# Performance work log

Measured on AMD Instinct MI355X. Metric: run time of the kernel, lower is better.

## Reference

```python
import jax, jax.numpy as jnp
import numpy as np

H, C = 4, 32            # num_heads, hidden_channels per head
HC = H * C
SLOPE_ATT = 0.2         # GATv2Conv negative_slope default
SLOPE_OUT = 0.01        # F.leaky_relu default

N_HOST, N_VM, N_JOB, N_SWITCH = 50000, 100000, 200000, 5000
IN_DIM = 64
E_HS, E_VH, E_JV = 200000, 400000, 800000


def _gatv2(x_src, x_dst, Wl, bl, Wr, br, att, bias, src, dst, n_dst):
    # PyG GATv2Conv (bipartite): lin_l on source, lin_r on destination
    xl = (x_src @ Wl + bl).reshape(-1, H, C)             # [Ns,H,C]
    xr = (x_dst @ Wr + br).reshape(-1, H, C)             # [Nd,H,C]
    e = jax.nn.leaky_relu(xl[src] + xr[dst], SLOPE_ATT)  # [E,H,C]
    logits = jnp.einsum('ehc,hc->eh', e, att)            # [E,H]
    m = jax.ops.segment_max(logits, dst, num_segments=n_dst)
    ex = jnp.exp(logits - m[dst])
    denom = jax.ops.segment_sum(ex, dst, num_segments=n_dst)
    alpha = ex / denom[dst]                              # scatter-softmax grouped by dst
    out = jax.ops.segment_sum(xl[src] * alpha[..., None], dst, num_segments=n_dst)
    return out.reshape(n_dst, HC) + bias, alpha


def setup_inputs() -> dict:
    key = jax.random.key(0)
    ks = iter(jax.random.split(key, 64))
    f32 = jnp.float32
    def randn(shape, scale=1.0):
        return jax.random.normal(next(ks), shape, dtype=f32) * scale
    sw = 1.0 / np.sqrt(IN_DIM)
    sa = 1.0 / np.sqrt(C)
    inp = {
        'x_host': randn((N_HOST, IN_DIM)),
        'x_vm': randn((N_VM, IN_DIM)),
        'x_job': randn((N_JOB, IN_DIM)),
        'x_switch': randn((N_SWITCH, IN_DIM)),
        'e_hs_src': jax.random.randint(next(ks), (E_HS,), 0, N_HOST),
        'e_hs_dst': jax.random.randint(next(ks), (E_HS,), 0, N_SWITCH),
        'e_vh_src': jax.random.randint(next(ks), (E_VH,), 0, N_VM),
        'e_vh_dst': jax.random.randint(next(ks), (E_VH,), 0, N_HOST),
        'e_jv_src': jax.random.randint(next(ks), (E_JV,), 0, N_JOB),
        'e_jv_dst': jax.random.randint(next(ks), (E_JV,), 0, N_VM),
    }
    for rel in ('hs', 'vh', 'jv'):
        inp['Wl_' + rel] = randn((IN_DIM, HC), sw)
        inp['bl_' + rel] = jnp.zeros((HC,), f32)
        inp['Wr_' + rel] = randn((IN_DIM, HC), sw)
        inp['br_' + rel] = jnp.zeros((HC,), f32)
        inp['att_' + rel] = randn((H, C), sa)
        inp['bias_' + rel] = jnp.zeros((HC,), f32)
    for nt in ('host', 'vm', 'job', 'switch'):
        inp['W_' + nt] = randn((HC, 1), 1.0 / np.sqrt(HC))
        inp['b_' + nt] = jnp.zeros((1,), f32)
    return inp


def reference(x_host, x_vm, x_job, x_switch,
              e_hs_src, e_hs_dst, e_vh_src, e_vh_dst, e_jv_src, e_jv_dst,
              Wl_hs, bl_hs, Wr_hs, br_hs, att_hs, bias_hs,
              Wl_vh, bl_vh, Wr_vh, br_vh, att_vh, bias_vh,
              Wl_jv, bl_jv, Wr_jv, br_jv, att_jv, bias_jv,
              W_host, b_host, W_vm, b_vm, W_job, b_job, W_switch, b_switch):
    out_switch, a_hs = _gatv2(x_host, x_switch, Wl_hs, bl_hs, Wr_hs, br_hs,
                              att_hs, bias_hs, e_hs_src, e_hs_dst, x_switch.shape[0])
    out_host, a_vh = _gatv2(x_vm, x_host, Wl_vh, bl_vh, Wr_vh, br_vh,
                            att_vh, bias_vh, e_vh_src, e_vh_dst, x_host.shape[0])
    out_vm, a_jv = _gatv2(x_job, x_vm, Wl_jv, bl_jv, Wr_jv, br_jv,
                          att_jv, bias_jv, e_jv_src, e_jv_dst, x_vm.shape[0])
    # each dst type receives exactly one relation; stack+sum is identity here
    h_host = jax.nn.leaky_relu(out_host, SLOPE_OUT)
    h_vm = jax.nn.leaky_relu(out_vm, SLOPE_OUT)
    h_switch = jax.nn.leaky_relu(out_switch, SLOPE_OUT)
    h_job = jnp.zeros((x_job.shape[0], HC), x_job.dtype)  # job has no incoming edges
    s_host = jax.nn.sigmoid(h_host @ W_host + b_host)
    s_vm = jax.nn.sigmoid(h_vm @ W_vm + b_vm)
    s_job = jax.nn.sigmoid(h_job @ W_job + b_job)
    s_switch = jax.nn.sigmoid(h_switch @ W_switch + b_switch)
    scores = jnp.concatenate([s_host, s_vm, s_job, s_switch], axis=0)
    return scores, a_hs, a_vh, a_jv
```

## Files before the change

kernel.cpp:

```cpp
#include <hip/hip_runtime.h>
#include <hip/hip_fp16.h>


#define SLOPE_ATT 0.2f
#define SLOPE_OUT 0.01f

typedef _Float16 half8_t __attribute__((ext_vector_type(8)));
typedef _Float16 v2h_t __attribute__((ext_vector_type(2)));
typedef float float4_t __attribute__((ext_vector_type(4)));

__device__ __forceinline__ float dot8(half8_t a, half8_t b, float acc) {
    v2h_t a0 = __builtin_shufflevector(a, a, 0, 1);
    v2h_t a1 = __builtin_shufflevector(a, a, 2, 3);
    v2h_t a2 = __builtin_shufflevector(a, a, 4, 5);
    v2h_t a3 = __builtin_shufflevector(a, a, 6, 7);
    v2h_t b0 = __builtin_shufflevector(b, b, 0, 1);
    v2h_t b1 = __builtin_shufflevector(b, b, 2, 3);
    v2h_t b2 = __builtin_shufflevector(b, b, 4, 5);
    v2h_t b3 = __builtin_shufflevector(b, b, 6, 7);
    acc = __builtin_amdgcn_fdot2(a0, b0, acc, false);
    acc = __builtin_amdgcn_fdot2(a1, b1, acc, false);
    acc = __builtin_amdgcn_fdot2(a2, b2, acc, false);
    acc = __builtin_amdgcn_fdot2(a3, b3, acc, false);
    return acc;
}

struct WSrc { const float* W[6]; };

__global__ __launch_bounds__(256) void init_wt_kernel(
    int* __restrict__ head, int ptot, WSrc wsrc, __half* __restrict__ Wt) {
    int i = blockIdx.x * 256 + threadIdx.x;
    if (i < ptot) {
        head[i] = -1;
    } else {
        int r = i - ptot;
        if (r < 6 * 8192) {
            int j = r >> 13;
            int rr = r & 8191;
            int n = rr >> 6, k = rr & 63;
            Wt[r] = (__half)wsrc.W[j][k * 128 + n];
        }
    }
}

__device__ __forceinline__ void gemm_tile_mfma(
    const float* __restrict__ X, const __half* __restrict__ Wt,
    const float* __restrict__ bb, __half* __restrict__ Y,
    int M, int block_row, __half (*sY)[16][136]) {
    const int lane = threadIdx.x & 63;
    const int wv = threadIdx.x >> 6;
    const int m0 = block_row + wv * 16;
    const int mr = lane & 15;
    const int quad = lane >> 4;
    const int gr = m0 + mr;
    const bool valid = gr < M;

    half8_t a0 = {}, a1 = {};
    float4 xa = {}, xb = {}, xc = {}, xd = {};
    if (valid) {
        const float4* xp = (const float4*)(X + (size_t)gr * 64 + quad * 8);
        xa = xp[0]; xb = xp[1];
        const float4* xq = (const float4*)(X + (size_t)gr * 64 + 32 + quad * 8);
        xc = xq[0]; xd = xq[1];
    }

    half8_t wb0[8], wb1[8];
    float bv[8];
#pragma unroll
    for (int t = 0; t < 8; t++) {
        const __half* wb = Wt + ((size_t)(t * 16 + mr)) * 64 + quad * 8;
        wb0[t] = *(const half8_t*)wb;
        wb1[t] = *(const half8_t*)(wb + 32);
        bv[t] = bb[t * 16 + mr];
    }

    a0[0] = (_Float16)xa.x; a0[1] = (_Float16)xa.y;
    a0[2] = (_Float16)xa.z; a0[3] = (_Float16)xa.w;
    a0[4] = (_Float16)xb.x; a0[5] = (_Float16)xb.y;
    a0[6] = (_Float16)xb.z; a0[7] = (_Float16)xb.w;
    a1[0] = (_Float16)xc.x; a1[1] = (_Float16)xc.y;
    a1[2] = (_Float16)xc.z; a1[3] = (_Float16)xc.w;
    a1[4] = (_Float16)xd.x; a1[5] = (_Float16)xd.y;
    a1[6] = (_Float16)xd.z; a1[7] = (_Float16)xd.w;

#pragma unroll
    for (int t = 0; t < 8; t++) {
        float4_t c = {0.f, 0.f, 0.f, 0.f};
        c = __builtin_amdgcn_mfma_f32_16x16x32_f16(a0, wb0[t], c, 0, 0, 0);
        c = __builtin_amdgcn_mfma_f32_16x16x32_f16(a1, wb1[t], c, 0, 0, 0);
        int ocol = t * 16 + mr;
        int lrow = quad * 4;
#pragma unroll
        for (int r = 0; r < 4; r++)
            sY[wv][lrow + r][ocol] = (__half)(c[r] + bv[t]);
    }

    const int rl = lane >> 4;
    const int c8 = (lane & 15) * 8;
#pragma unroll
    for (int i = 0; i < 4; i++) {
        int row = i * 4 + rl;
        int gr2 = m0 + row;
        if (gr2 < M) {
            half8_t v = *(const half8_t*)&sY[wv][row][c8];
            *(half8_t*)&Y[(size_t)gr2 * 128 + c8] = v;
        }
    }
}

__device__ __forceinline__ void link_work(
    int linkId, int linkBlocks,
    const int* __restrict__ d0, const int* __restrict__ s0,
    const int* __restrict__ d1, const int* __restrict__ s1,
    const int* __restrict__ d2, const int* __restrict__ s2,
    int* __restrict__ head, int2* __restrict__ nxt,
    int E0, int E1, int E2, int pb1, int pb2) {
    int i = linkId * 256 + threadIdx.x;
    int Etot = E0 + E1 + E2;
    int stride = linkBlocks * 256;
    for (; i < Etot; i += stride) {
        int le, slot; const int* sp;
        if (i < E0)           { le = i;           slot = d0[le];       sp = s0; }
        else if (i < E0 + E1) { le = i - E0;      slot = pb1 + d1[le]; sp = s1; }
        else                  { le = i - E0 - E1; slot = pb2 + d2[le]; sp = s2; }
        int old = atomicExch(&head[slot], le);
        nxt[i] = make_int2(old, sp[le]);
    }
}

struct GemmJobs {
    const float* X[6]; const float* b[6]; __half* Y[6];
    int M[6]; int base[7];
};

__global__ __launch_bounds__(256) void mega_gemm_link_kernel(
    GemmJobs j, const __half* __restrict__ Wt, int s, int L,
    const int* __restrict__ d0, const int* __restrict__ s0,
    const int* __restrict__ d1, const int* __restrict__ s1,
    const int* __restrict__ d2, const int* __restrict__ s2,
    int* __restrict__ head, int2* __restrict__ nxt,
    int E0, int E1, int E2, int pb1, int pb2) {
    __shared__ __half sY[4][16][136];
    int b = blockIdx.x;
    int q = b / s;
    bool onGridline = (b - q * s) == 0;
    if (onGridline && q < L) {
        link_work(q, L, d0, s0, d1, s1, d2, s2, head, nxt, E0, E1, E2, pb1, pb2);
    } else {
        int before = q + (onGridline ? 0 : 1);
        if (before > L) before = L;
        int g = b - before;
        int k = 0;
        while (g >= j.base[k + 1]) k++;
        gemm_tile_mfma(j.X[k], Wt + (size_t)k * 8192, j.b[k], j.Y[k], j.M[k],
                       (g - j.base[k]) * 64, sY);
    }
}

struct AggJob {
    const __half* xl; const __half* xr; const float* att;
    const int* head; const int2* nxt;
    float* ex; float* dn;
    const float* bias; const float* Wn; const float* bn; float* scores;
    int Nd;
};
struct AggJobs { AggJob r[3]; int base[4]; };

__global__ __launch_bounds__(256) void agg3_kernel(AggJobs aj) {
    int b = blockIdx.x;
    int k = 0;
    while (b >= aj.base[k + 1]) k++;
    AggJob J = aj.r[k];

    const int l = threadIdx.x & 63;
    const int wv = threadIdx.x >> 6;
    const int li = l & 7;
    const int g = l >> 3;
    const int dbase = ((b - aj.base[k]) * 4 + wv) * 8;
    const int d = dbase + g;
    if (dbase >= J.Nd) return;
    const bool dok = d < J.Nd;
    const int h = li >> 1;

    half8_t xr0 = {}, xr1 = {};
    if (dok) {
        const half8_t* xrp = (const half8_t*)(J.xr + (size_t)d * 128) + li * 2;
        xr0 = xrp[0]; xr1 = xrp[1];
    }
    half8_t at0, at1;
    {
        const float* ap = J.att + li * 16;
#pragma unroll
        for (int i = 0; i < 8; i++) {
            at0[i] = (_Float16)ap[i];
            at1[i] = (_Float16)ap[8 + i];
        }
    }
    const half8_t sl8 = {(_Float16)SLOPE_ATT, (_Float16)SLOPE_ATT,
                         (_Float16)SLOPE_ATT, (_Float16)SLOPE_ATT,
                         (_Float16)SLOPE_ATT, (_Float16)SLOPE_ATT,
                         (_Float16)SLOPE_ATT, (_Float16)SLOPE_ATT};

    float acc[16] = {};
    float ssum = 0.f;

    int e = dok ? J.head[d] : -1;
    const bool any = (e >= 0);

    while (__any(e >= 0)) {
        bool act = (e >= 0);
        int2 ns = act ? J.nxt[e] : make_int2(-1, 0);
        half8_t x0 = {}, x1 = {};
        if (act) {
            const half8_t* xp = (const half8_t*)(J.xl + (size_t)ns.y * 128) + li * 2;
            x0 = xp[0]; x1 = xp[1];
        }
        if (act) {
            half8_t v0 = x0 + xr0;
            half8_t v1 = x1 + xr1;
            half8_t lk0 = __builtin_elementwise_max(v0, v0 * sl8);
            half8_t lk1 = __builtin_elementwise_max(v1, v1 * sl8);
            float p = dot8(lk1, at1, dot8(lk0, at0, 0.f));
            p += __shfl_xor(p, 1);
            float w = __expf(p);
            if ((li & 1) == 0) J.ex[(size_t)e * 4 + h] = w;
            ssum += w;
#pragma unroll
            for (int i = 0; i < 8; i++) {
                acc[i]     += w * (float)x0[i];
                acc[8 + i] += w * (float)x1[i];
            }
        }
        e = act ? ns.x : -1;
    }

    if (dok && (li & 1) == 0) J.dn[(size_t)d * 4 + h] = ssum;

    float rr = any ? 1.f / ssum : 0.f;
    float pr = 0.f;
    if (dok) {
        const float* bp = J.bias + li * 16;
        const float* wp = J.Wn + li * 16;
#pragma unroll
        for (int i = 0; i < 16; i++) {
            float o = acc[i] * rr + bp[i];
            o = o > 0.f ? o : SLOPE_OUT * o;
            pr += o * wp[i];
        }
    }
    pr += __shfl_xor(pr, 1);
    pr += __shfl_xor(pr, 2);
    pr += __shfl_xor(pr, 4);
    if (dok && li == 0)
        J.scores[d] = 1.f / (1.f + __expf(-(pr + J.bn[0])));
}

__global__ __launch_bounds__(256) void alpha_job_kernel(
    float* __restrict__ ex,
    const int* __restrict__ d0, const int* __restrict__ d1,
    const int* __restrict__ d2,
    const float* __restrict__ dn,
    int E0, int E1, int E2, int pb1, int pb2, int ab,
    const float* __restrict__ bjob, float* __restrict__ sjob, int NJ) {
    int b = blockIdx.x;
    if (b < ab) {
        int i = b * 256 + threadIdx.x;
        int tot = (E0 + E1 + E2) * 4;
        if (i >= tot) return;
        int e = i >> 2, h = i & 3;
        int d;
        if (e < E0)           d = d0[e];
        else if (e < E0 + E1) d = pb1 + d1[e - E0];
        else                  d = pb2 + d2[e - E0 - E1];
        ex[i] = ex[i] / dn[(size_t)d * 4 + h];
    } else {
        int i = (b - ab) * 256 + threadIdx.x;
        if (i < NJ) sjob[i] = 1.f / (1.f + __expf(-bjob[0]));
    }
}


extern "C" void kernel_launch(void* const* d_in, const int* in_sizes, int n_in,
                              void* d_out, int out_size, void* d_ws, size_t ws_size,
                              hipStream_t stream) {
    const float* x_host   = (const float*)d_in[0];
    const float* x_vm     = (const float*)d_in[1];
    const float* x_job    = (const float*)d_in[2];
    const float* x_switch = (const float*)d_in[3];
    const int* e_hs_src = (const int*)d_in[4];
    const int* e_hs_dst = (const int*)d_in[5];
    const int* e_vh_src = (const int*)d_in[6];
    const int* e_vh_dst = (const int*)d_in[7];
    const int* e_jv_src = (const int*)d_in[8];
    const int* e_jv_dst = (const int*)d_in[9];
    const float* Wl_hs = (const float*)d_in[10];
    const float* bl_hs = (const float*)d_in[11];
    const float* Wr_hs = (const float*)d_in[12];
    const float* br_hs = (const float*)d_in[13];
    const float* att_hs = (const float*)d_in[14];
    const float* bias_hs = (const float*)d_in[15];
    const float* Wl_vh = (const float*)d_in[16];
    const float* bl_vh = (const float*)d_in[17];
    const float* Wr_vh = (const float*)d_in[18];
    const float* br_vh = (const float*)d_in[19];
    const float* att_vh = (const float*)d_in[20];
    const float* bias_vh = (const float*)d_in[21];
    const float* Wl_jv = (const float*)d_in[22];
    const float* bl_jv = (const float*)d_in[23];
    const float* Wr_jv = (const float*)d_in[24];
    const float* br_jv = (const float*)d_in[25];
    const float* att_jv = (const float*)d_in[26];
    const float* bias_jv = (const float*)d_in[27];
    const float* W_host   = (const float*)d_in[28];
    const float* b_host   = (const float*)d_in[29];
    const float* W_vm     = (const float*)d_in[30];
    const float* b_vm     = (const float*)d_in[31];
    const float* W_job    = (const float*)d_in[32];
    const float* b_job    = (const float*)d_in[33];
    const float* W_switch = (const float*)d_in[34];
    const float* b_switch = (const float*)d_in[35];

    const int NH  = in_sizes[0] / 64;
    const int NV  = in_sizes[1] / 64;
    const int NJ  = in_sizes[2] / 64;
    const int NSW = in_sizes[3] / 64;
    const int EHS = in_sizes[4];
    const int EVH = in_sizes[6];
    const int EJV = in_sizes[8];
    const int Etot = EHS + EVH + EJV;

    float* out = (float*)d_out;
    float* s_host = out;
    float* s_vm = out + NH;
    float* s_job = out + NH + NV;
    float* s_sw = out + NH + NV + NJ;
    float* a_hs = out + NH + NV + NJ + NSW;
    float* a_vh = a_hs + (size_t)EHS * 4;
    float* a_jv = a_vh + (size_t)EVH * 4;

    const int pb1 = ((NSW + 255) / 256) * 256;
    const int pb2 = pb1 + ((NH + 255) / 256) * 256;
    const int ptot = pb2 + ((NV + 255) / 256) * 256;

    float* ws = (float*)d_ws;
    int2* nxt_all = (int2*)ws;
    int* head_all = (int*)(nxt_all + Etot);
    float* dn_all = (float*)(head_all + ptot);
    __half* Wt    = (__half*)(dn_all + (size_t)ptot * 4);
    __half* mats  = Wt + 6 * 8192;
    __half* xl_hs = mats;
    __half* xr_hs = xl_hs + (size_t)NH * 128;
    __half* xl_vh = xr_hs + (size_t)NSW * 128;
    __half* xr_vh = xl_vh + (size_t)NV * 128;
    __half* xl_jv = xr_vh + (size_t)NH * 128;
    __half* xr_jv = xl_jv + (size_t)NJ * 128;

    {
        WSrc w;
        w.W[0] = Wl_hs; w.W[1] = Wr_hs; w.W[2] = Wl_vh;
        w.W[3] = Wr_vh; w.W[4] = Wl_jv; w.W[5] = Wr_jv;
        int tot = ptot + 6 * 8192;
        init_wt_kernel<<<(tot + 255) / 256, 256, 0, stream>>>(head_all, ptot, w, Wt);
    }

    {
        GemmJobs j;
        const float* Xs[6] = {x_host, x_switch, x_vm, x_host, x_job, x_vm};
        const float* bs[6] = {bl_hs, br_hs, bl_vh, br_vh, bl_jv, br_jv};
        __half* Ys[6] = {xl_hs, xr_hs, xl_vh, xr_vh, xl_jv, xr_jv};
        int Ms[6] = {NH, NSW, NV, NH, NJ, NV};
        int base = 0;
        for (int k = 0; k < 6; k++) {
            j.X[k] = Xs[k]; j.b[k] = bs[k]; j.Y[k] = Ys[k]; j.M[k] = Ms[k];
            j.base[k] = base;
            base += (Ms[k] + 63) / 64;
        }
        j.base[6] = base;
        int L = 3072;
        int T = base + L;
        int s = T / L; if (s < 1) s = 1;
        mega_gemm_link_kernel<<<T, 256, 0, stream>>>(
            j, Wt, s, L, e_hs_dst, e_hs_src, e_vh_dst, e_vh_src,
            e_jv_dst, e_jv_src, head_all, nxt_all, EHS, EVH, EJV, pb1, pb2);
    }

    {
        AggJobs aj;
        aj.r[0] = {xl_hs, xr_hs, att_hs, head_all + 0, nxt_all + 0,
                   a_hs, dn_all + 0,
                   bias_hs, W_switch, b_switch, s_sw, NSW};
        aj.r[1] = {xl_vh, xr_vh, att_vh, head_all + pb1, nxt_all + EHS,
                   a_vh, dn_all + (size_t)pb1 * 4,
                   bias_vh, W_host, b_host, s_host, NH};
        aj.r[2] = {xl_jv, xr_jv, att_jv, head_all + pb2, nxt_all + (EHS + EVH),
                   a_jv, dn_all + (size_t)pb2 * 4,
                   bias_jv, W_vm, b_vm, s_vm, NV};
        aj.base[0] = 0;
        aj.base[1] = (NSW + 31) / 32;
        aj.base[2] = aj.base[1] + (NH + 31) / 32;
        aj.base[3] = aj.base[2] + (NV + 31) / 32;
        agg3_kernel<<<aj.base[3], 256, 0, stream>>>(aj);
    }

    {
        int ab = (Etot * 4 + 255) / 256;
        int jb = (NJ + 255) / 256;
        alpha_job_kernel<<<ab + jb, 256, 0, stream>>>(
            a_hs, e_hs_dst, e_vh_dst, e_jv_dst, dn_all,
            EHS, EVH, EJV, pb1, pb2, ab, b_job, s_job, NJ);
    }
}
```

Before: 392.3 us.

## Make GEMM blocks persistent with register-held weights and prefetched X tiles

The fused GEMM+link kernel now launches a fixed pool of persistent GEMM blocks, split across the six projection jobs in proportion to their row-tile counts, plus a fixed block range for the linked-list build. It replaces the one-tile-per-block launch with interleaved link blocks. Each GEMM block loads its weight fragments and bias into registers once and loops over row tiles, prefetching the next tile's X rows while computing the current one. This removes per-tile weight reloads and block launch overhead. The cost is less parallelism per job and possible load imbalance between the link and GEMM partitions.

```diff
diff --git a/kernel.cpp b/kernel.cpp
--- a/kernel.cpp
+++ b/kernel.cpp
@@ -39,71 +39,6 @@
             int rr = r & 8191;
             int n = rr >> 6, k = rr & 63;
             Wt[r] = (__half)wsrc.W[j][k * 128 + n];
-        }
-    }
-}
-
-__device__ __forceinline__ void gemm_tile_mfma(
-    const float* __restrict__ X, const __half* __restrict__ Wt,
-    const float* __restrict__ bb, __half* __restrict__ Y,
-    int M, int block_row, __half (*sY)[16][136]) {
-    const int lane = threadIdx.x & 63;
-    const int wv = threadIdx.x >> 6;
-    const int m0 = block_row + wv * 16;
-    const int mr = lane & 15;
-    const int quad = lane >> 4;
-    const int gr = m0 + mr;
-    const bool valid = gr < M;
-
-    half8_t a0 = {}, a1 = {};
-    float4 xa = {}, xb = {}, xc = {}, xd = {};
-    if (valid) {
-        const float4* xp = (const float4*)(X + (size_t)gr * 64 + quad * 8);
-        xa = xp[0]; xb = xp[1];
-        const float4* xq = (const float4*)(X + (size_t)gr * 64 + 32 + quad * 8);
-        xc = xq[0]; xd = xq[1];
-    }
-
-    half8_t wb0[8], wb1[8];
-    float bv[8];
-#pragma unroll
-    for (int t = 0; t < 8; t++) {
-        const __half* wb = Wt + ((size_t)(t * 16 + mr)) * 64 + quad * 8;
-        wb0[t] = *(const half8_t*)wb;
-        wb1[t] = *(const half8_t*)(wb + 32);
-        bv[t] = bb[t * 16 + mr];
-    }
-
-    a0[0] = (_Float16)xa.x; a0[1] = (_Float16)xa.y;
-    a0[2] = (_Float16)xa.z; a0[3] = (_Float16)xa.w;
-    a0[4] = (_Float16)xb.x; a0[5] = (_Float16)xb.y;
-    a0[6] = (_Float16)xb.z; a0[7] = (_Float16)xb.w;
-    a1[0] = (_Float16)xc.x; a1[1] = (_Float16)xc.y;
-    a1[2] = (_Float16)xc.z; a1[3] = (_Float16)xc.w;
-    a1[4] = (_Float16)xd.x; a1[5] = (_Float16)xd.y;
-    a1[6] = (_Float16)xd.z; a1[7] = (_Float16)xd.w;
-
-#pragma unroll
-    for (int t = 0; t < 8; t++) {
-        float4_t c = {0.f, 0.f, 0.f, 0.f};
-        c = __builtin_amdgcn_mfma_f32_16x16x32_f16(a0, wb0[t], c, 0, 0, 0);
-        c = __builtin_amdgcn_mfma_f32_16x16x32_f16(a1, wb1[t], c, 0, 0, 0);
-        int ocol = t * 16 + mr;
-        int lrow = quad * 4;
-#pragma unroll
-        for (int r = 0; r < 4; r++)
-            sY[wv][lrow + r][ocol] = (__half)(c[r] + bv[t]);
-    }
-
-    const int rl = lane >> 4;
-    const int c8 = (lane & 15) * 8;
-#pragma unroll
-    for (int i = 0; i < 4; i++) {
-        int row = i * 4 + rl;
-        int gr2 = m0 + row;
-        if (gr2 < M) {
-            half8_t v = *(const half8_t*)&sY[wv][row][c8];
-            *(half8_t*)&Y[(size_t)gr2 * 128 + c8] = v;
         }
     }
 }
@@ -130,11 +65,11 @@
 
 struct GemmJobs {
     const float* X[6]; const float* b[6]; __half* Y[6];
-    int M[6]; int base[7];
+    int M[6]; int pbase[7];
 };
 
 __global__ __launch_bounds__(256) void mega_gemm_link_kernel(
-    GemmJobs j, const __half* __restrict__ Wt, int s, int L,
+    GemmJobs j, const __half* __restrict__ Wt, int LB,
     const int* __restrict__ d0, const int* __restrict__ s0,
     const int* __restrict__ d1, const int* __restrict__ s1,
     const int* __restrict__ d2, const int* __restrict__ s2,
@@ -142,18 +77,97 @@
     int E0, int E1, int E2, int pb1, int pb2) {
     __shared__ __half sY[4][16][136];
     int b = blockIdx.x;
-    int q = b / s;
-    bool onGridline = (b - q * s) == 0;
-    if (onGridline && q < L) {
-        link_work(q, L, d0, s0, d1, s1, d2, s2, head, nxt, E0, E1, E2, pb1, pb2);
-    } else {
-        int before = q + (onGridline ? 0 : 1);
-        if (before > L) before = L;
-        int g = b - before;
-        int k = 0;
-        while (g >= j.base[k + 1]) k++;
-        gemm_tile_mfma(j.X[k], Wt + (size_t)k * 8192, j.b[k], j.Y[k], j.M[k],
-                       (g - j.base[k]) * 64, sY);
+    if (b < LB) {
+        link_work(b, LB, d0, s0, d1, s1, d2, s2, head, nxt, E0, E1, E2, pb1, pb2);
+        return;
+    }
+    int bb = b - LB;
+    int k = 0;
+    while (bb >= j.pbase[k + 1]) k++;
+    const int p = bb - j.pbase[k];
+    const int gb = j.pbase[k + 1] - j.pbase[k];
+    const int M = j.M[k];
+    const int nb = (M + 63) >> 6;
+    if (p >= nb) return;
+    const float* __restrict__ X = j.X[k];
+    __half* __restrict__ Y = j.Y[k];
+    const float* __restrict__ bb_ = j.b[k];
+    const __half* __restrict__ W = Wt + (size_t)k * 8192;
+
+    const int lane = threadIdx.x & 63;
+    const int wv = threadIdx.x >> 6;
+    const int mr = lane & 15;
+    const int quad = lane >> 4;
+
+    half8_t wb0[8], wb1[8];
+    float bv[8];
+#pragma unroll
+    for (int t = 0; t < 8; t++) {
+        const __half* wp = W + ((size_t)(t * 16 + mr)) * 64 + quad * 8;
+        wb0[t] = *(const half8_t*)wp;
+        wb1[t] = *(const half8_t*)(wp + 32);
+        bv[t] = bb_[t * 16 + mr];
+    }
+
+    float4 xc0 = {}, xc1 = {}, xc2 = {}, xc3 = {};
+    {
+        int gr = p * 64 + wv * 16 + mr;
+        if (gr < M) {
+            const float4* xp = (const float4*)(X + (size_t)gr * 64 + quad * 8);
+            xc0 = xp[0]; xc1 = xp[1];
+            const float4* xq = (const float4*)(X + (size_t)gr * 64 + 32 + quad * 8);
+            xc2 = xq[0]; xc3 = xq[1];
+        }
+    }
+
+    for (int t = p; t < nb; t += gb) {
+        int tn = t + gb;
+        float4 xn0 = {}, xn1 = {}, xn2 = {}, xn3 = {};
+        if (tn < nb) {
+            int gr = tn * 64 + wv * 16 + mr;
+            if (gr < M) {
+                const float4* xp = (const float4*)(X + (size_t)gr * 64 + quad * 8);
+                xn0 = xp[0]; xn1 = xp[1];
+                const float4* xq = (const float4*)(X + (size_t)gr * 64 + 32 + quad * 8);
+                xn2 = xq[0]; xn3 = xq[1];
+            }
+        }
+
+        half8_t a0, a1;
+        a0[0] = (_Float16)xc0.x; a0[1] = (_Float16)xc0.y;
+        a0[2] = (_Float16)xc0.z; a0[3] = (_Float16)xc0.w;
+        a0[4] = (_Float16)xc1.x; a0[5] = (_Float16)xc1.y;
+        a0[6] = (_Float16)xc1.z; a0[7] = (_Float16)xc1.w;
+        a1[0] = (_Float16)xc2.x; a1[1] = (_Float16)xc2.y;
+        a1[2] = (_Float16)xc2.z; a1[3] = (_Float16)xc2.w;
+        a1[4] = (_Float16)xc3.x; a1[5] = (_Float16)xc3.y;
+        a1[6] = (_Float16)xc3.z; a1[7] = (_Float16)xc3.w;
+
+        const int m0 = t * 64 + wv * 16;
+#pragma unroll
+        for (int tt = 0; tt < 8; tt++) {
+            float4_t c = {0.f, 0.f, 0.f, 0.f};
+            c = __builtin_amdgcn_mfma_f32_16x16x32_f16(a0, wb0[tt], c, 0, 0, 0);
+            c = __builtin_amdgcn_mfma_f32_16x16x32_f16(a1, wb1[tt], c, 0, 0, 0);
+            int ocol = tt * 16 + mr;
+            int lrow = quad * 4;
+#pragma unroll
+            for (int r = 0; r < 4; r++)
+                sY[wv][lrow + r][ocol] = (__half)(c[r] + bv[tt]);
+        }
+
+        const int c8 = mr * 8;
+#pragma unroll
+        for (int i = 0; i < 4; i++) {
+            int row = i * 4 + quad;
+            int gr2 = m0 + row;
+            if (gr2 < M) {
+                half8_t v = *(const half8_t*)&sY[wv][row][c8];
+                *(half8_t*)&Y[(size_t)gr2 * 128 + c8] = v;
+            }
+        }
+
+        xc0 = xn0; xc1 = xn1; xc2 = xn2; xc3 = xn3;
     }
 }
 
@@ -369,18 +383,21 @@
         const float* bs[6] = {bl_hs, br_hs, bl_vh, br_vh, bl_jv, br_jv};
         __half* Ys[6] = {xl_hs, xr_hs, xl_vh, xr_vh, xl_jv, xr_jv};
         int Ms[6] = {NH, NSW, NV, NH, NJ, NV};
-        int base = 0;
+        int nbk[6]; long long total_nb = 0;
+        for (int k = 0; k < 6; k++) { nbk[k] = (Ms[k] + 63) / 64; total_nb += nbk[k]; }
+        const int GBTOT = 1664;
+        const int LB = 384;
+        int pb = 0;
         for (int k = 0; k < 6; k++) {
             j.X[k] = Xs[k]; j.b[k] = bs[k]; j.Y[k] = Ys[k]; j.M[k] = Ms[k];
-            j.base[k] = base;
-            base += (Ms[k] + 63) / 64;
-        }
-        j.base[6] = base;
-        int L = 3072;
-        int T = base + L;
-        int s = T / L; if (s < 1) s = 1;
-        mega_gemm_link_kernel<<<T, 256, 0, stream>>>(
-            j, Wt, s, L, e_hs_dst, e_hs_src, e_vh_dst, e_vh_src,
+            j.pbase[k] = pb;
+            int gb = (int)(((long long)GBTOT * nbk[k]) / total_nb);
+            if (gb < 1) gb = 1;
+            pb += gb;
+        }
+        j.pbase[6] = pb;
+        mega_gemm_link_kernel<<<LB + pb, 256, 0, stream>>>(
+            j, Wt, LB, e_hs_dst, e_hs_src, e_vh_dst, e_vh_src,
             e_jv_dst, e_jv_src, head_all, nxt_all, EHS, EVH, EJV, pb1, pb2);
     }
 
```

New measurement: 367.5 us. 1.07x faster.
